# Performance work log

Hardware: AMD Instinct MI355X
Metric: run time of the kernel (lower is better)

Reference implementation:

```python
import jax, jax.numpy as jnp
import numpy as np


def setup_inputs() -> dict:
    key = jax.random.key(0)
    k1, k2 = jax.random.split(key)
    pred = jax.random.normal(k1, (4, 8192, 3), dtype=jnp.float32)
    gt = jax.random.normal(k2, (4, 8192, 3), dtype=jnp.float32)
    return {"pred": pred, "gt": gt}


def reference(pred, gt):
    # pairwise squared distances: [B, N, M]
    diff = pred[:, :, None, :] - gt[:, None, :, :]
    distances = jnp.sum(diff ** 2, axis=-1)
    pred_to_gt = jnp.min(distances, axis=2)  # [B, N]
    gt_to_pred = jnp.min(distances, axis=1)  # [B, M]
    return jnp.mean(pred_to_gt) + jnp.mean(gt_to_pred)
```

## Files before the change

### kernel.cpp

```cpp
#include <hip/hip_runtime.h>
#include <math.h>


typedef _Float16 half8 __attribute__((ext_vector_type(8)));
typedef float f32x16 __attribute__((ext_vector_type(16)));

#define NPTS   8192
#define CLOUD  32768
#define NQ_TOT 65536
#define TT     1024
#define NTC    8

#define QPACK_OFF  0
#define TPACK_OFF  (2u * 1024 * 1024)
#define PART_OFF   (4u * 1024 * 1024)

__global__ __launch_bounds__(256) void pack_kernel(
    const float* __restrict__ pred, const float* __restrict__ gt,
    char* __restrict__ ws, float* __restrict__ out) {
  int i = blockIdx.x * 256 + threadIdx.x;
  int cloud = i >> 15, j = i & (CLOUD - 1);
  const float* src = cloud ? gt : pred;
  float x = src[3 * j], y = src[3 * j + 1], z = src[3 * j + 2];
  float s = x * x + y * y + z * z;

  _Float16 xh = (_Float16)x; _Float16 xl = (_Float16)(x - (float)xh);
  _Float16 yh = (_Float16)y; _Float16 yl = (_Float16)(y - (float)yh);
  _Float16 zh = (_Float16)z; _Float16 zl = (_Float16)(z - (float)zh);
  _Float16 sh = (_Float16)s; _Float16 sl = (_Float16)(s - (float)sh);
  _Float16 Xh = (_Float16)(-2.f * (float)xh), Xl = (_Float16)(-2.f * (float)xl);
  _Float16 Yh = (_Float16)(-2.f * (float)yh), Yl = (_Float16)(-2.f * (float)yl);
  _Float16 Zh = (_Float16)(-2.f * (float)zh), Zl = (_Float16)(-2.f * (float)zl);
  _Float16 one = (_Float16)1.0f;

  half8 q0 = {xh, xh, xl, xl, yh, yh, yl, yl};
  half8 q1 = {zh, zh, zl, zl, one, one, sh, sl};
  half8 t0 = {Xh, Xl, Xh, Xl, Yh, Yl, Yh, Yl};
  half8 t1 = {Zh, Zl, Zh, Zl, sh, sl, one, one};

  half8* qp = (half8*)(ws + QPACK_OFF);
  half8* tp = (half8*)(ws + TPACK_OFF);
  qp[2 * i] = q0; qp[2 * i + 1] = q1;
  tp[2 * i] = t0; tp[2 * i + 1] = t1;
  if (i == 0) out[0] = 0.f;
}

__device__ __forceinline__ float min_fold(float m, const f32x16& d) {
  float a = fminf(fminf(d[0], d[1]), d[2]);
  float b = fminf(fminf(d[3], d[4]), d[5]);
  float c = fminf(fminf(d[6], d[7]), d[8]);
  float e = fminf(fminf(d[9], d[10]), d[11]);
  float f = fminf(fminf(d[12], d[13]), d[14]);
  float g = fminf(fminf(a, b), c);
  float h = fminf(fminf(e, f), d[15]);
  return fminf(m, fminf(g, h));
}

__global__ __launch_bounds__(256, 4) void chamfer_mfma(
    const char* __restrict__ ws_in, float* __restrict__ partial) {
  __shared__ __align__(16) char lds[TT * 32];
  int bid = blockIdx.x;
  int tc   = bid & (NTC - 1);
  int qblk = (bid >> 3) & 31;
  int b    = (bid >> 8) & 3;
  int dir  = bid >> 10;
  int t = threadIdx.x, lane = t & 63, wave = t >> 6;

  const float4* src4 = (const float4*)(ws_in + TPACK_OFF) +
      (size_t)((dir ? 0 : CLOUD) + b * NPTS + tc * TT) * 2;
  float4* dst4 = (float4*)lds;
  #pragma unroll
  for (int k = 0; k < 8; ++k) dst4[t + 256 * k] = src4[t + 256 * k];

  int qlocal = qblk * 256 + wave * 64;
  const char* qbase = ws_in + QPACK_OFF +
      (size_t)((dir ? CLOUD : 0) + b * NPTS + qlocal) * 32;
  half8 bq0 = *(const half8*)(qbase + (lane & 31) * 32 + (lane >> 5) * 16);
  half8 bq1 = *(const half8*)(qbase + 32 * 32 + (lane & 31) * 32 + (lane >> 5) * 16);
  __syncthreads();

  const char* abase = lds + (lane & 31) * 32 + (lane >> 5) * 16;
  float m0 = INFINITY, m1 = INFINITY;
  f32x16 zero = {};
  #pragma unroll 4
  for (int g = 0; g < TT / 32; ++g) {
    half8 a = *(const half8*)(abase + g * 1024);
    f32x16 d0 = __builtin_amdgcn_mfma_f32_32x32x16_f16(a, bq0, zero, 0, 0, 0);
    f32x16 d1 = __builtin_amdgcn_mfma_f32_32x32x16_f16(a, bq1, zero, 0, 0, 0);
    m0 = min_fold(m0, d0);
    m1 = min_fold(m1, d1);
  }
  m0 = fminf(m0, __shfl_xor(m0, 32, 64));
  m1 = fminf(m1, __shfl_xor(m1, 32, 64));

  if (lane < 32) {
    size_t qi = (size_t)dir * CLOUD + b * NPTS + qlocal + lane;
    partial[(size_t)tc * NQ_TOT + qi]      = fmaxf(m0, 0.f);
    partial[(size_t)tc * NQ_TOT + qi + 32] = fmaxf(m1, 0.f);
  }
}

__global__ __launch_bounds__(256) void reduce_kernel(
    const float* __restrict__ partial, float* __restrict__ out) {
  __shared__ float wsum[4];
  int i = blockIdx.x * 256 + threadIdx.x;
  float m = partial[i];
  #pragma unroll
  for (int tc = 1; tc < NTC; ++tc)
    m = fminf(m, partial[(size_t)tc * NQ_TOT + i]);
  float acc = m * (1.0f / 32768.0f);
  #pragma unroll
  for (int off = 32; off > 0; off >>= 1) acc += __shfl_down(acc, off, 64);
  int wid = threadIdx.x >> 6;
  if ((threadIdx.x & 63) == 0) wsum[wid] = acc;
  __syncthreads();
  if (threadIdx.x == 0) atomicAdd(out, wsum[0] + wsum[1] + wsum[2] + wsum[3]);
}

extern "C" void kernel_launch(void* const* d_in, const int* in_sizes, int n_in,
                              void* d_out, int out_size, void* d_ws, size_t ws_size,
                              hipStream_t stream) {
  const float* pred = (const float*)d_in[0];
  const float* gt   = (const float*)d_in[1];
  float* out = (float*)d_out;
  char* ws = (char*)d_ws;
  float* partial = (float*)(ws + PART_OFF);

  pack_kernel<<<256, 256, 0, stream>>>(pred, gt, ws, out);
  chamfer_mfma<<<2048, 256, 0, stream>>>(ws, partial);
  reduce_kernel<<<256, 256, 0, stream>>>(partial, out);
}
```

Before: 83.81 us.

## Fuse point packing into chamfer kernel and halve target tile size

Removes the separate pack kernel: each block now reads raw float xyz for its target tile and query points, splits them into fp16 hi/lo parts in-kernel, and writes the packed targets straight into LDS. The target tile shrinks from 1024 to 512 points, so the grid doubles to 4096 blocks and the partial-minimum buffer and reduce pass cover 16 tiles instead of 8. This drops one launch and the workspace round-trip, at the cost of redundant per-block packing arithmetic and twice the partial-buffer traffic in the reduction.

```diff
diff --git a/kernel.cpp b/kernel.cpp
--- a/kernel.cpp
+++ b/kernel.cpp
@@ -8,41 +8,11 @@
 #define NPTS   8192
 #define CLOUD  32768
 #define NQ_TOT 65536
-#define TT     1024
-#define NTC    8
+#define TT     512
+#define NTC    16
 
-#define QPACK_OFF  0
-#define TPACK_OFF  (2u * 1024 * 1024)
-#define PART_OFF   (4u * 1024 * 1024)
-
-__global__ __launch_bounds__(256) void pack_kernel(
-    const float* __restrict__ pred, const float* __restrict__ gt,
-    char* __restrict__ ws, float* __restrict__ out) {
-  int i = blockIdx.x * 256 + threadIdx.x;
-  int cloud = i >> 15, j = i & (CLOUD - 1);
-  const float* src = cloud ? gt : pred;
-  float x = src[3 * j], y = src[3 * j + 1], z = src[3 * j + 2];
-  float s = x * x + y * y + z * z;
-
-  _Float16 xh = (_Float16)x; _Float16 xl = (_Float16)(x - (float)xh);
-  _Float16 yh = (_Float16)y; _Float16 yl = (_Float16)(y - (float)yh);
-  _Float16 zh = (_Float16)z; _Float16 zl = (_Float16)(z - (float)zh);
-  _Float16 sh = (_Float16)s; _Float16 sl = (_Float16)(s - (float)sh);
-  _Float16 Xh = (_Float16)(-2.f * (float)xh), Xl = (_Float16)(-2.f * (float)xl);
-  _Float16 Yh = (_Float16)(-2.f * (float)yh), Yl = (_Float16)(-2.f * (float)yl);
-  _Float16 Zh = (_Float16)(-2.f * (float)zh), Zl = (_Float16)(-2.f * (float)zl);
-  _Float16 one = (_Float16)1.0f;
-
-  half8 q0 = {xh, xh, xl, xl, yh, yh, yl, yl};
-  half8 q1 = {zh, zh, zl, zl, one, one, sh, sl};
-  half8 t0 = {Xh, Xl, Xh, Xl, Yh, Yl, Yh, Yl};
-  half8 t1 = {Zh, Zl, Zh, Zl, sh, sl, one, one};
-
-  half8* qp = (half8*)(ws + QPACK_OFF);
-  half8* tp = (half8*)(ws + TPACK_OFF);
-  qp[2 * i] = q0; qp[2 * i + 1] = q1;
-  tp[2 * i] = t0; tp[2 * i + 1] = t1;
-  if (i == 0) out[0] = 0.f;
+__device__ __forceinline__ void split2(float v, _Float16& h, _Float16& l) {
+  h = (_Float16)v; l = (_Float16)(v - (float)h);
 }
 
 __device__ __forceinline__ float min_fold(float m, const f32x16& d) {
@@ -57,36 +27,56 @@
 }
 
 __global__ __launch_bounds__(256, 4) void chamfer_mfma(
-    const char* __restrict__ ws_in, float* __restrict__ partial) {
-  __shared__ __align__(16) char lds[TT * 32];
+    const float* __restrict__ pred, const float* __restrict__ gt,
+    float* __restrict__ partial, float* __restrict__ out) {
+  __shared__ __align__(16) half8 lds[TT * 2];
   int bid = blockIdx.x;
   int tc   = bid & (NTC - 1);
-  int qblk = (bid >> 3) & 31;
-  int b    = (bid >> 8) & 3;
-  int dir  = bid >> 10;
+  int qblk = (bid >> 4) & 31;
+  int b    = (bid >> 9) & 3;
+  int dir  = bid >> 11;
+  const float* qsrc = dir ? gt : pred;
+  const float* tsrc = dir ? pred : gt;
   int t = threadIdx.x, lane = t & 63, wave = t >> 6;
+  if (bid == 0 && t == 0) out[0] = 0.f;
 
-  const float4* src4 = (const float4*)(ws_in + TPACK_OFF) +
-      (size_t)((dir ? 0 : CLOUD) + b * NPTS + tc * TT) * 2;
-  float4* dst4 = (float4*)lds;
+  const float* tb = tsrc + (size_t)(b * NPTS + tc * TT) * 3;
+  for (int k = t; k < TT; k += 256) {
+    float x = tb[3 * k], y = tb[3 * k + 1], z = tb[3 * k + 2];
+    float s = x * x + y * y + z * z;
+    _Float16 xh, xl, yh, yl, zh, zl, sh, sl;
+    split2(x, xh, xl); split2(y, yh, yl); split2(z, zh, zl); split2(s, sh, sl);
+    _Float16 Xh = (_Float16)(-2.f * (float)xh), Xl = (_Float16)(-2.f * (float)xl);
+    _Float16 Yh = (_Float16)(-2.f * (float)yh), Yl = (_Float16)(-2.f * (float)yl);
+    _Float16 Zh = (_Float16)(-2.f * (float)zh), Zl = (_Float16)(-2.f * (float)zl);
+    _Float16 one = (_Float16)1.0f;
+    lds[2 * k]     = (half8){Xh, Xl, Xh, Xl, Yh, Yl, Yh, Yl};
+    lds[2 * k + 1] = (half8){Zh, Zl, Zh, Zl, sh, sl, one, one};
+  }
+
+  const float* qb = qsrc + (size_t)(b * NPTS + qblk * 256 + wave * 64) * 3;
+  half8 bq[2];
   #pragma unroll
-  for (int k = 0; k < 8; ++k) dst4[t + 256 * k] = src4[t + 256 * k];
-
-  int qlocal = qblk * 256 + wave * 64;
-  const char* qbase = ws_in + QPACK_OFF +
-      (size_t)((dir ? CLOUD : 0) + b * NPTS + qlocal) * 32;
-  half8 bq0 = *(const half8*)(qbase + (lane & 31) * 32 + (lane >> 5) * 16);
-  half8 bq1 = *(const half8*)(qbase + 32 * 32 + (lane & 31) * 32 + (lane >> 5) * 16);
+  for (int h = 0; h < 2; ++h) {
+    int qi = (lane & 31) + 32 * h;
+    float x = qb[3 * qi], y = qb[3 * qi + 1], z = qb[3 * qi + 2];
+    float s = x * x + y * y + z * z;
+    _Float16 xh, xl, yh, yl, zh, zl, sh, sl;
+    split2(x, xh, xl); split2(y, yh, yl); split2(z, zh, zl); split2(s, sh, sl);
+    _Float16 one = (_Float16)1.0f;
+    bq[h] = (lane < 32) ? (half8){xh, xh, xl, xl, yh, yh, yl, yl}
+                        : (half8){zh, zh, zl, zl, one, one, sh, sl};
+  }
   __syncthreads();
 
-  const char* abase = lds + (lane & 31) * 32 + (lane >> 5) * 16;
+  int arow = 2 * (lane & 31) + (lane >> 5);
   float m0 = INFINITY, m1 = INFINITY;
   f32x16 zero = {};
-  #pragma unroll 4
+  #pragma unroll 2
   for (int g = 0; g < TT / 32; ++g) {
-    half8 a = *(const half8*)(abase + g * 1024);
-    f32x16 d0 = __builtin_amdgcn_mfma_f32_32x32x16_f16(a, bq0, zero, 0, 0, 0);
-    f32x16 d1 = __builtin_amdgcn_mfma_f32_32x32x16_f16(a, bq1, zero, 0, 0, 0);
+    half8 a = lds[arow + g * 64];
+    f32x16 d0 = __builtin_amdgcn_mfma_f32_32x32x16_f16(a, bq[0], zero, 0, 0, 0);
+    f32x16 d1 = __builtin_amdgcn_mfma_f32_32x32x16_f16(a, bq[1], zero, 0, 0, 0);
     m0 = min_fold(m0, d0);
     m1 = min_fold(m1, d1);
   }
@@ -94,7 +84,7 @@
   m1 = fminf(m1, __shfl_xor(m1, 32, 64));
 
   if (lane < 32) {
-    size_t qi = (size_t)dir * CLOUD + b * NPTS + qlocal + lane;
+    size_t qi = (size_t)dir * CLOUD + b * NPTS + qblk * 256 + wave * 64 + (lane & 31);
     partial[(size_t)tc * NQ_TOT + qi]      = fmaxf(m0, 0.f);
     partial[(size_t)tc * NQ_TOT + qi + 32] = fmaxf(m1, 0.f);
   }
@@ -123,10 +113,8 @@
   const float* pred = (const float*)d_in[0];
   const float* gt   = (const float*)d_in[1];
   float* out = (float*)d_out;
-  char* ws = (char*)d_ws;
-  float* partial = (float*)(ws + PART_OFF);
+  float* partial = (float*)d_ws;
 
-  pack_kernel<<<256, 256, 0, stream>>>(pred, gt, ws, out);
-  chamfer_mfma<<<2048, 256, 0, stream>>>(ws, partial);
+  chamfer_mfma<<<4096, 256, 0, stream>>>(pred, gt, partial, out);
   reduce_kernel<<<256, 256, 0, stream>>>(partial, out);
 }
```

New measurement: 78.97 us. 5.8% less time.
